# Optimization experiments

Measured on AMD Instinct MI355X. Metric: run time of the kernel, lower is better.

The kernel has to match this reference:

```python
import math
import jax, jax.numpy as jnp
import numpy as np

D_MODEL = 512
NHEAD = 8
D_HEAD = D_MODEL // NHEAD
TEMP = 0.8
B, LQ, LK = 16, 512, 1024
NEG = -1.0e9


def setup_inputs() -> dict:
    key = jax.random.key(0)
    ks = jax.random.split(key, 12)
    s = 1.0 / math.sqrt(D_MODEL)
    return {
        "Q_src": jax.random.normal(ks[0], (B, LQ, D_MODEL), jnp.float32),
        "KV_src": jax.random.normal(ks[1], (B, LK, D_MODEL), jnp.float32),
        "key_gate": jax.random.uniform(ks[2], (B, LK), jnp.float32, 1e-3, 1.0),
        "key_padding_mask": jax.random.randint(ks[3], (B, LK), 0, 2, jnp.int32),
        "Wq": jax.random.normal(ks[4], (D_MODEL, D_MODEL), jnp.float32) * s,
        "bq": jnp.zeros((D_MODEL,), jnp.float32),
        "Wk": jax.random.normal(ks[5], (D_MODEL, D_MODEL), jnp.float32) * s,
        "bk": jnp.zeros((D_MODEL,), jnp.float32),
        "Wv": jax.random.normal(ks[6], (D_MODEL, D_MODEL), jnp.float32) * s,
        "bv": jnp.zeros((D_MODEL,), jnp.float32),
        "Wo": jax.random.normal(ks[7], (D_MODEL, D_MODEL), jnp.float32) * s,
        "bo": jnp.zeros((D_MODEL,), jnp.float32),
    }


def reference(Q_src, KV_src, key_gate, key_padding_mask, Wq, bq, Wk, bk, Wv, bv, Wo, bo):
    b, lq, _ = Q_src.shape
    lk = KV_src.shape[1]
    # projections -> [B, H, L, Dh]
    q = (Q_src @ Wq + bq).reshape(b, lq, NHEAD, D_HEAD).transpose(0, 2, 1, 3)
    k = (KV_src @ Wk + bk).reshape(b, lk, NHEAD, D_HEAD).transpose(0, 2, 1, 3)
    v = (KV_src @ Wv + bv).reshape(b, lk, NHEAD, D_HEAD).transpose(0, 2, 1, 3)
    # scores with log-gate bias [B, H, Lq, Lk]
    logits = jnp.einsum("bhqd,bhkd->bhqk", q, k) / math.sqrt(D_HEAD)
    logits = logits + jnp.log(key_gate)[:, None, None, :]
    pad = (key_padding_mask == 0)[:, None, None, :]
    logits = jnp.where(pad, NEG, logits) / TEMP
    attn = jax.nn.softmax(logits, axis=-1)
    ctx = jnp.einsum("bhqk,bhkd->bhqd", attn, v)
    ctx = ctx.transpose(0, 2, 1, 3).reshape(b, lq, D_MODEL)
    return ctx @ Wo + bo
```

## Files before the change

kernel.cpp:

```cpp
#include <hip/hip_runtime.h>
#include <math.h>

typedef __bf16 bf16;
typedef __bf16 bf16x8 __attribute__((ext_vector_type(8)));
typedef __bf16 bf16x4 __attribute__((ext_vector_type(4)));
typedef __bf16 bf16x2 __attribute__((ext_vector_type(2)));
typedef float  f32x4  __attribute__((ext_vector_type(4)));
typedef unsigned int uint;

#define SCQ 0.15625f

#define VMC(n) asm volatile("s_waitcnt vmcnt(" #n ")" ::: "memory")
#define BARR do { __builtin_amdgcn_s_barrier(); __builtin_amdgcn_sched_barrier(0); } while (0)

__device__ __forceinline__ void gload16(const void* g, void* l) {
  __builtin_amdgcn_global_load_lds((const __attribute__((address_space(1))) void*)g,
                                   (__attribute__((address_space(3))) void*)l, 16, 0, 0);
}

__device__ __forceinline__ uint pk2(float a, float b) {
  bf16x2 t = {(bf16)a, (bf16)b};
  return __builtin_bit_cast(uint, t);
}

union V8 { bf16x8 v; bf16x4 h[2]; uint u[4]; };

__global__ void prep_k(const float* __restrict__ Wq, const float* __restrict__ Wk,
                       const float* __restrict__ Wv, const float* __restrict__ Wo,
                       bf16* __restrict__ Tq, bf16* __restrict__ Tkv, bf16* __restrict__ To,
                       const float* __restrict__ gate, const int* __restrict__ mask,
                       float* __restrict__ gfac) {
  const int bid = blockIdx.x, tid = threadIdx.x;
  if (bid < 256) {
    const int w = bid >> 6, t = bid & 63;
    const float* W = (w == 0) ? Wq : (w == 1) ? Wk : (w == 2) ? Wv : Wo;
    bf16* T = (w == 0) ? Tq : (w == 3) ? To : Tkv;
    const int ro = (w == 2) ? 512 : 0;
    const int k0 = (t >> 3) * 64, n0 = (t & 7) * 64;
    __shared__ bf16 tl[64][72];
#pragma unroll
    for (int i = 0; i < 16; i++) {
      int s = i * 256 + tid;
      int r = s >> 6, c = s & 63;
      tl[r][c] = (bf16)W[(size_t)(k0 + r) * 512 + n0 + c];
    }
    __syncthreads();
#pragma unroll
    for (int i = 0; i < 16; i++) {
      int s = i * 256 + tid;
      int r = s >> 6, c = s & 63;
      T[(size_t)(ro + n0 + r) * 512 + k0 + c] = tl[c][r];
    }
  } else {
    int i = (bid - 256) * 256 + tid;
    gfac[i] = mask[i] ? __expf(1.25f * __logf(gate[i])) : 0.0f;
  }
}

__global__ void conv_k(const float* __restrict__ s, bf16* __restrict__ d) {
  const size_t i = ((size_t)blockIdx.x * 256 + threadIdx.x) * 8;
  f32x4 a = *(const f32x4*)(s + i);
  f32x4 b = *(const f32x4*)(s + i + 4);
  bf16x8 o = {(bf16)a[0], (bf16)a[1], (bf16)a[2], (bf16)a[3],
              (bf16)b[0], (bf16)b[1], (bf16)b[2], (bf16)b[3]};
  *(bf16x8*)(d + i) = o;
}

__global__ __launch_bounds__(512, 2) void gemm_kv8(
    const bf16* __restrict__ A, const bf16* __restrict__ Bt,
    const float* __restrict__ kb, const float* __restrict__ vb,
    const float* __restrict__ gfac, bf16* __restrict__ K_out, bf16* __restrict__ V_out) {
  const int tid = threadIdx.x, w = tid >> 6, l = tid & 63;
  const int lg = l >> 4, lr = l & 15;
  const int bid = (int)(blockIdx.x & 7) * 32 + (int)(blockIdx.x >> 3);
  const int bm = (bid >> 2) * 256;
  const int bn = (bid & 3) * 256;
  const int wm = w >> 2, wn = w & 3;

  __shared__ __align__(16) bf16 AB[2][16384];

  const int lrow = l >> 2;
  const int cs = (l & 3) ^ ((l >> 3) & 3);

  f32x4 acc[8][4];
#pragma unroll
  for (int i = 0; i < 8; i++)
#pragma unroll
    for (int j = 0; j < 4; j++) acc[i][j] = (f32x4){0.f, 0.f, 0.f, 0.f};

  auto stA = [&](int p, int u, int kt) {
    const int rb = (w >> 2) * 128 + u * 64 + (w & 3) * 16;
    gload16(A + (size_t)(bm + rb + lrow) * 512 + kt * 32 + cs * 8, &AB[p][rb * 32]);
  };
  auto stB = [&](int p, int u, int kt) {
    const int rb = (w >> 1) * 64 + u * 32 + (w & 1) * 16;
    gload16(Bt + (size_t)(bn + rb + lrow) * 512 + kt * 32 + cs * 8, &AB[p][8192 + rb * 32]);
  };

  bf16x8 aA[4], bb0[2], bb1[2];
#define RDA(p, mh)                                                                   \
  _Pragma("unroll") for (int m2 = 0; m2 < 4; m2++) {                                 \
    const int row = wm * 128 + (mh) * 64 + m2 * 16 + lr;                             \
    aA[m2] = *(const bf16x8*)(&AB[p][row * 32 + ((lg ^ ((row >> 1) & 3)) * 8)]);     \
  }
#define RDB(p, nh, dst)                                                              \
  _Pragma("unroll") for (int n2 = 0; n2 < 2; n2++) {                                 \
    const int row = wn * 64 + (nh) * 32 + n2 * 16 + lr;                              \
    dst[n2] = *(const bf16x8*)(&AB[p][8192 + row * 32 + ((lg ^ ((row >> 1) & 3)) * 8)]); \
  }
#define MM(mh, nh, bbv)                                                              \
  __builtin_amdgcn_s_setprio(1);                                                     \
  _Pragma("unroll") for (int m2 = 0; m2 < 4; m2++)                                   \
  _Pragma("unroll") for (int n2 = 0; n2 < 2; n2++)                                   \
    acc[(mh) * 4 + m2][(nh) * 2 + n2] =                                              \
        __builtin_amdgcn_mfma_f32_16x16x32_bf16(aA[m2], bbv[n2],                     \
                                                acc[(mh) * 4 + m2][(nh) * 2 + n2], 0, 0, 0); \
  __builtin_amdgcn_s_setprio(0);

  stA(0, 0, 0); stB(0, 0, 0); stA(0, 1, 0); stB(0, 1, 0);
  stA(1, 0, 1); stB(1, 0, 1);
  VMC(4);
  BARR;

  for (int i = 0; i < 8; ++i) {
    const bool last = (i == 7);
    const int k1 = 2 * i + 1, k2 = 2 * i + 2, k3 = 2 * i + 3;
    stA(1, 1, k1); stB(1, 1, k1);
    RDA(0, 0); RDB(0, 0, bb0);
    MM(0, 0, bb0);
    VMC(4); BARR;
    RDB(0, 1, bb1);
    MM(0, 1, bb1);
    BARR;
    if (!last) stA(0, 0, k2);
    RDA(0, 1);
    MM(1, 0, bb0);
    BARR;
    if (!last) stB(0, 0, k2);
    MM(1, 1, bb1);
    if (last) { VMC(2); } else { VMC(4); }
    BARR;
    if (!last) { stA(0, 1, k2); stB(0, 1, k2); }
    RDA(1, 0); RDB(1, 0, bb0);
    MM(0, 0, bb0);
    if (last) { VMC(0); } else { VMC(4); }
    BARR;
    RDB(1, 1, bb1);
    MM(0, 1, bb1);
    BARR;
    if (!last) stA(1, 0, k3);
    RDA(1, 1);
    MM(1, 0, bb0);
    BARR;
    if (!last) stB(1, 0, k3);
    MM(1, 1, bb1);
    VMC(4); BARR;
  }
#undef RDA
#undef RDB
#undef MM

  if (bn < 512) {
#pragma unroll
    for (int mf = 0; mf < 8; mf++) {
#pragma unroll
      for (int nf = 0; nf < 4; nf++) {
        f32x4 c = acc[mf][nf];
        const int n = bn + wn * 64 + nf * 16 + lr;
        const int m0 = bm + wm * 128 + mf * 16 + lg * 4;
        const float bias = kb[n];
#pragma unroll
        for (int r = 0; r < 4; r++) K_out[(size_t)(m0 + r) * 512 + n] = (bf16)(c[r] + bias);
      }
    }
  } else {
#pragma unroll
    for (int mf = 0; mf < 8; mf++) {
#pragma unroll
      for (int nf = 0; nf < 4; nf++) {
        f32x4 c = acc[mf][nf];
        const int n = bn + wn * 64 + nf * 16 + lr;
        const int m0 = bm + wm * 128 + mf * 16 + lg * 4;
        const int nn = n - 512;
        const int hh = nn >> 6, dd = nn & 63;
        const int bb = m0 >> 10, key = m0 & 1023;
        const int u = key & 31;
        const int keyp = (key & ~31) + ((u & 15) >> 2) * 8 + ((u >> 4) & 1) * 4;
        const float bias = vb[nn];
        f32x4 g4 = *(const f32x4*)(gfac + m0);
        bf16x4 w4 = {(bf16)((c[0] + bias) * g4[0]), (bf16)((c[1] + bias) * g4[1]),
                     (bf16)((c[2] + bias) * g4[2]), (bf16)((c[3] + bias) * g4[3])};
        *(bf16x4*)(V_out + ((size_t)((bb * 8 + hh) * 64 + dd)) * 1024 + keyp) = w4;
      }
    }
  }
}

template <int BM, int OM, int NT, int CHUNK>
__global__ __launch_bounds__(256) void gemm_k(
    const bf16* __restrict__ A, const bf16* __restrict__ Bt,
    const float* __restrict__ b0, void* __restrict__ C0, float scale) {
  constexpr int MF = BM / 32;
  const int tid = threadIdx.x, w = tid >> 6, l = tid & 63;
  const int lg = l >> 4, lr = l & 15;
  const int bid = (int)(blockIdx.x & 7) * CHUNK + (int)(blockIdx.x >> 3);
  const int bm = (bid / NT) * BM;
  const int bn = (bid % NT) * 128;
  const int wr = (w >> 1) * (BM / 2), wc = (w & 1) * 64;
  __shared__ __align__(16) bf16 As[2][BM][64];
  __shared__ __align__(16) bf16 Bs[2][128][64];
  const int srow8 = l >> 3;
  const int c8 = (l & 7) ^ srow8;
  const int xorlr = (lr & 7);

  f32x4 acc[MF][4];
#pragma unroll
  for (int i = 0; i < MF; i++)
#pragma unroll
    for (int j = 0; j < 4; j++) acc[i][j] = (f32x4){0.f, 0.f, 0.f, 0.f};

  auto stage = [&](int buf, int k0) {
#pragma unroll
    for (int i = 0; i < MF; i++)
      gload16(A + (size_t)(bm + i * 32 + w * 8 + srow8) * 512 + k0 + c8 * 8,
              &As[buf][i * 32 + w * 8][0]);
#pragma unroll
    for (int i = 0; i < 4; i++)
      gload16(Bt + (size_t)(bn + i * 32 + w * 8 + srow8) * 512 + k0 + c8 * 8,
              &Bs[buf][i * 32 + w * 8][0]);
  };

  stage(0, 0);
  for (int t = 0; t < 8; ++t) {
    const int buf = t & 1;
    __syncthreads();
    if (t < 7) stage(buf ^ 1, (t + 1) * 64);
#pragma unroll
    for (int kk = 0; kk < 2; kk++) {
      bf16x8 af[MF], bfr[4];
#pragma unroll
      for (int mf = 0; mf < MF; mf++)
        af[mf] = *(const bf16x8*)(&As[buf][wr + mf * 16 + lr][((kk * 4 + lg) ^ xorlr) * 8]);
#pragma unroll
      for (int nf = 0; nf < 4; nf++)
        bfr[nf] = *(const bf16x8*)(&Bs[buf][wc + nf * 16 + lr][((kk * 4 + lg) ^ xorlr) * 8]);
#pragma unroll
      for (int mf = 0; mf < MF; mf++)
#pragma unroll
        for (int nf = 0; nf < 4; nf++)
          acc[mf][nf] = __builtin_amdgcn_mfma_f32_16x16x32_bf16(af[mf], bfr[nf], acc[mf][nf], 0, 0, 0);
    }
  }

#pragma unroll
  for (int mf = 0; mf < MF; mf++) {
#pragma unroll
    for (int nf = 0; nf < 4; nf++) {
      f32x4 c = acc[mf][nf];
      const int n = bn + wc + nf * 16 + lr;
      const int m0 = bm + wr + mf * 16 + lg * 4;
      const float bias = b0[n];
      if constexpr (OM == 0) {
        bf16* C = (bf16*)C0;
#pragma unroll
        for (int r = 0; r < 4; r++) C[(size_t)(m0 + r) * 512 + n] = (bf16)((c[r] + bias) * scale);
      } else {
        float* C = (float*)C0;
#pragma unroll
        for (int r = 0; r < 4; r++) C[(size_t)(m0 + r) * 512 + n] = c[r] + bias;
      }
    }
  }
}

__global__ __launch_bounds__(512) void attn_k(
    const bf16* __restrict__ Q, const bf16* __restrict__ Kb,
    const bf16* __restrict__ Vt, const float* __restrict__ gfac,
    bf16* __restrict__ ctx) {
  const int tid = threadIdx.x, w = tid >> 6, l = tid & 63;
  const int lg = l >> 4, lr = l & 15;
  const int bid = (int)(blockIdx.x & 7) * 32 + (int)(blockIdx.x >> 3);
  const int qb = bid & 1, h = (bid >> 1) & 7, b = bid >> 4;
  const int q0 = qb * 256;

  __shared__ __align__(16) bf16 Ks[2][64][64];
  __shared__ __align__(16) bf16 Vs[2][64][64];

  bf16x8 qf[2][2];
#pragma unroll
  for (int s = 0; s < 2; s++) {
    const bf16* qp = Q + (size_t)(b * 512 + q0 + w * 32 + s * 16 + lr) * 512 + h * 64;
    qf[s][0] = *(const bf16x8*)(qp + lg * 8);
    qf[s][1] = *(const bf16x8*)(qp + 32 + lg * 8);
  }

  f32x4 o[2][4];
#pragma unroll
  for (int s = 0; s < 2; s++)
#pragma unroll
    for (int i = 0; i < 4; i++) o[s][i] = (f32x4){0.f, 0.f, 0.f, 0.f};
  float m_r[2] = {-3.0e38f, -3.0e38f}, l_p[2] = {0.f, 0.f};
  const float* gfb = gfac + b * 1024;

  const int srow = w * 8 + (l >> 3);
  const int c8g = (l & 7) ^ ((l >> 3) & 7);
  const bf16* Kbase = Kb + ((size_t)b * 1024) * 512 + h * 64 + c8g * 8;
  const bf16* Vbase = Vt + (((size_t)(b * 8 + h)) * 64 + srow) * 1024 + c8g * 8;

  gload16(Kbase + (size_t)srow * 512, &Ks[0][w * 8][0]);
  gload16(Vbase, &Vs[0][w * 8][0]);

  for (int t = 0; t < 16; ++t) {
    const int buf = t & 1;
    __syncthreads();
    if (t < 15) {
      gload16(Kbase + (size_t)((t + 1) * 64 + srow) * 512, &Ks[buf ^ 1][w * 8][0]);
      gload16(Vbase + (t + 1) * 64, &Vs[buf ^ 1][w * 8][0]);
    }
    f32x4 gv[4];
#pragma unroll
    for (int f = 0; f < 4; f++) gv[f] = *(const f32x4*)(gfb + t * 64 + f * 16 + lg * 4);

    f32x4 s4[2][4];
    __builtin_amdgcn_s_setprio(1);
#pragma unroll
    for (int f = 0; f < 4; f++) {
      const int row = f * 16 + lr;
      const bf16x8 k0 = *(const bf16x8*)(&Ks[buf][row][(lg ^ (row & 7)) * 8]);
      const bf16x8 k1 = *(const bf16x8*)(&Ks[buf][row][((4 + lg) ^ (row & 7)) * 8]);
#pragma unroll
      for (int s = 0; s < 2; s++) {
        f32x4 z = (f32x4){0.f, 0.f, 0.f, 0.f};
        z = __builtin_amdgcn_mfma_f32_16x16x32_bf16(k0, qf[s][0], z, 0, 0, 0);
        s4[s][f] = __builtin_amdgcn_mfma_f32_16x16x32_bf16(k1, qf[s][1], z, 0, 0, 0);
      }
    }
    __builtin_amdgcn_s_setprio(0);

    V8 pb[2][2];
#pragma unroll
    for (int s = 0; s < 2; s++) {
      float mx = fmaxf(fmaxf(fmaxf(s4[s][0][0], s4[s][0][1]), fmaxf(s4[s][0][2], s4[s][0][3])),
                       fmaxf(fmaxf(s4[s][1][0], s4[s][1][1]), fmaxf(s4[s][1][2], s4[s][1][3])));
      mx = fmaxf(mx, fmaxf(fmaxf(fmaxf(s4[s][2][0], s4[s][2][1]), fmaxf(s4[s][2][2], s4[s][2][3])),
                           fmaxf(fmaxf(s4[s][3][0], s4[s][3][1]), fmaxf(s4[s][3][2], s4[s][3][3]))));
      mx = fmaxf(mx, __shfl_xor(mx, 16));
      mx = fmaxf(mx, __shfl_xor(mx, 32));
      if (!__all(mx <= m_r[s] + 8.f)) {
        const float mn = fmaxf(m_r[s], mx);
        const float al = __expf(m_r[s] - mn);
        m_r[s] = mn;
        l_p[s] *= al;
#pragma unroll
        for (int od = 0; od < 4; od++)
#pragma unroll
          for (int r = 0; r < 4; r++) o[s][od][r] *= al;
      }
      float p[4][4];
#pragma unroll
      for (int f = 0; f < 4; f++)
#pragma unroll
        for (int r = 0; r < 4; r++) p[f][r] = __expf(s4[s][f][r] - m_r[s]);
#pragma unroll
      for (int f = 0; f < 4; f++)
#pragma unroll
        for (int r = 0; r < 4; r++) l_p[s] = fmaf(p[f][r], gv[f][r], l_p[s]);
      pb[s][0].u[0] = pk2(p[0][0], p[0][1]); pb[s][0].u[1] = pk2(p[0][2], p[0][3]);
      pb[s][0].u[2] = pk2(p[1][0], p[1][1]); pb[s][0].u[3] = pk2(p[1][2], p[1][3]);
      pb[s][1].u[0] = pk2(p[2][0], p[2][1]); pb[s][1].u[1] = pk2(p[2][2], p[2][3]);
      pb[s][1].u[2] = pk2(p[3][0], p[3][1]); pb[s][1].u[3] = pk2(p[3][2], p[3][3]);
    }

    __builtin_amdgcn_s_setprio(1);
#pragma unroll
    for (int od = 0; od < 4; od++) {
      const int row = od * 16 + lr;
      const bf16x8 va0 = *(const bf16x8*)(&Vs[buf][row][(lg ^ (row & 7)) * 8]);
      const bf16x8 va1 = *(const bf16x8*)(&Vs[buf][row][((4 + lg) ^ (row & 7)) * 8]);
#pragma unroll
      for (int s = 0; s < 2; s++) {
        o[s][od] = __builtin_amdgcn_mfma_f32_16x16x32_bf16(va0, pb[s][0].v, o[s][od], 0, 0, 0);
        o[s][od] = __builtin_amdgcn_mfma_f32_16x16x32_bf16(va1, pb[s][1].v, o[s][od], 0, 0, 0);
      }
    }
    __builtin_amdgcn_s_setprio(0);
  }

#pragma unroll
  for (int s = 0; s < 2; s++) {
    float lp = l_p[s];
    lp += __shfl_xor(lp, 16);
    lp += __shfl_xor(lp, 32);
    const float inv = 1.0f / lp;
    bf16* cp = ctx + (size_t)(b * 512 + q0 + w * 32 + s * 16 + lr) * 512 + h * 64;
#pragma unroll
    for (int od = 0; od < 4; od++)
#pragma unroll
      for (int r = 0; r < 4; r++) cp[od * 16 + lg * 4 + r] = (bf16)(o[s][od][r] * inv);
  }
}

extern "C" void kernel_launch(void* const* d_in, const int* in_sizes, int n_in,
                              void* d_out, int out_size, void* d_ws, size_t ws_size,
                              hipStream_t stream) {
  (void)in_sizes; (void)n_in; (void)out_size; (void)ws_size;
  const float* Q_src = (const float*)d_in[0];
  const float* KV_src = (const float*)d_in[1];
  const float* gate = (const float*)d_in[2];
  const int* mask = (const int*)d_in[3];
  const float* Wq = (const float*)d_in[4];
  const float* bq = (const float*)d_in[5];
  const float* Wk = (const float*)d_in[6];
  const float* bk = (const float*)d_in[7];
  const float* Wv = (const float*)d_in[8];
  const float* bv = (const float*)d_in[9];
  const float* Wo = (const float*)d_in[10];
  const float* bo = (const float*)d_in[11];
  float* out = (float*)d_out;

  char* ws = (char*)d_ws;
  size_t off = 0;
  auto alloc = [&](size_t bytes) {
    char* p = ws + off;
    off += (bytes + 255) & ~(size_t)255;
    return p;
  };
  bf16* Wtq = (bf16*)alloc(512 * 512 * 2);
  bf16* Btkv = (bf16*)alloc(1024 * 512 * 2);
  bf16* Wto = (bf16*)alloc(512 * 512 * 2);
  float* gfac = (float*)alloc(16384 * 4);
  bf16* Qsb = (bf16*)alloc((size_t)8192 * 512 * 2);
  bf16* KVb = (bf16*)alloc((size_t)16384 * 512 * 2);
  bf16* Qb = (bf16*)alloc((size_t)8192 * 512 * 2);
  bf16* Kb = (bf16*)alloc((size_t)16384 * 512 * 2);
  bf16* Vt = (bf16*)alloc((size_t)16384 * 512 * 2);
  bf16* Cx = KVb;

  prep_k<<<320, 256, 0, stream>>>(Wq, Wk, Wv, Wo, Wtq, Btkv, Wto, gate, mask, gfac);
  conv_k<<<2048, 256, 0, stream>>>(Q_src, Qsb);
  conv_k<<<4096, 256, 0, stream>>>(KV_src, KVb);
  gemm_kv8<<<256, 512, 0, stream>>>(KVb, Btkv, bk, bv, gfac, Kb, Vt);
  gemm_k<64, 0, 4, 64><<<512, 256, 0, stream>>>(Qsb, Wtq, bq, Qb, SCQ);
  attn_k<<<256, 512, 0, stream>>>(Qb, Kb, Vt, gfac, Cx);
  gemm_k<64, 2, 4, 64><<<512, 256, 0, stream>>>(Cx, Wto, bo, out, 1.0f);
}
```

Baseline: 98.05 us.

## Fuse conversion kernels into prep, triple-buffer GEMM and attention, use exp2 softmax

```diff
diff --git a/kernel.cpp b/kernel.cpp
--- a/kernel.cpp
+++ b/kernel.cpp
@@ -8,10 +8,16 @@
 typedef float  f32x4  __attribute__((ext_vector_type(4)));
 typedef unsigned int uint;
 
-#define SCQ 0.15625f
+#define SCQ2 0.22542110f
 
 #define VMC(n) asm volatile("s_waitcnt vmcnt(" #n ")" ::: "memory")
 #define BARR do { __builtin_amdgcn_s_barrier(); __builtin_amdgcn_sched_barrier(0); } while (0)
+
+#if __has_builtin(__builtin_amdgcn_exp2f)
+#define EXP2F __builtin_amdgcn_exp2f
+#else
+#define EXP2F exp2f
+#endif
 
 __device__ __forceinline__ void gload16(const void* g, void* l) {
   __builtin_amdgcn_global_load_lds((const __attribute__((address_space(1))) void*)g,
@@ -29,7 +35,9 @@
                        const float* __restrict__ Wv, const float* __restrict__ Wo,
                        bf16* __restrict__ Tq, bf16* __restrict__ Tkv, bf16* __restrict__ To,
                        const float* __restrict__ gate, const int* __restrict__ mask,
-                       float* __restrict__ gfac) {
+                       float* __restrict__ gfac,
+                       const float* __restrict__ Qs, const float* __restrict__ KVs,
+                       bf16* __restrict__ Qsb, bf16* __restrict__ KVb) {
   const int bid = blockIdx.x, tid = threadIdx.x;
   if (bid < 256) {
     const int w = bid >> 6, t = bid & 63;
@@ -51,19 +59,21 @@
       int r = s >> 6, c = s & 63;
       T[(size_t)(ro + n0 + r) * 512 + k0 + c] = tl[c][r];
     }
-  } else {
+  } else if (bid < 320) {
     int i = (bid - 256) * 256 + tid;
     gfac[i] = mask[i] ? __expf(1.25f * __logf(gate[i])) : 0.0f;
-  }
-}
-
-__global__ void conv_k(const float* __restrict__ s, bf16* __restrict__ d) {
-  const size_t i = ((size_t)blockIdx.x * 256 + threadIdx.x) * 8;
-  f32x4 a = *(const f32x4*)(s + i);
-  f32x4 b = *(const f32x4*)(s + i + 4);
-  bf16x8 o = {(bf16)a[0], (bf16)a[1], (bf16)a[2], (bf16)a[3],
-              (bf16)b[0], (bf16)b[1], (bf16)b[2], (bf16)b[3]};
-  *(bf16x8*)(d + i) = o;
+  } else {
+    const float* s;
+    bf16* d;
+    size_t i;
+    if (bid < 2368) { s = Qs; d = Qsb; i = ((size_t)(bid - 320) * 256 + tid) * 8; }
+    else            { s = KVs; d = KVb; i = ((size_t)(bid - 2368) * 256 + tid) * 8; }
+    f32x4 a = *(const f32x4*)(s + i);
+    f32x4 b = *(const f32x4*)(s + i + 4);
+    bf16x8 o = {(bf16)a[0], (bf16)a[1], (bf16)a[2], (bf16)a[3],
+                (bf16)b[0], (bf16)b[1], (bf16)b[2], (bf16)b[3]};
+    *(bf16x8*)(d + i) = o;
+  }
 }
 
 __global__ __launch_bounds__(512, 2) void gemm_kv8(
@@ -196,64 +206,64 @@
   }
 }
 
-template <int BM, int OM, int NT, int CHUNK>
-__global__ __launch_bounds__(256) void gemm_k(
+template <int OM, int NT, int CHUNK>
+__global__ __launch_bounds__(256, 2) void gemm_k(
     const bf16* __restrict__ A, const bf16* __restrict__ Bt,
     const float* __restrict__ b0, void* __restrict__ C0, float scale) {
-  constexpr int MF = BM / 32;
   const int tid = threadIdx.x, w = tid >> 6, l = tid & 63;
   const int lg = l >> 4, lr = l & 15;
   const int bid = (int)(blockIdx.x & 7) * CHUNK + (int)(blockIdx.x >> 3);
-  const int bm = (bid / NT) * BM;
+  const int bm = (bid / NT) * 64;
   const int bn = (bid % NT) * 128;
-  const int wr = (w >> 1) * (BM / 2), wc = (w & 1) * 64;
-  __shared__ __align__(16) bf16 As[2][BM][64];
-  __shared__ __align__(16) bf16 Bs[2][128][64];
-  const int srow8 = l >> 3;
-  const int c8 = (l & 7) ^ srow8;
-  const int xorlr = (lr & 7);
-
-  f32x4 acc[MF][4];
-#pragma unroll
-  for (int i = 0; i < MF; i++)
+  const int wr = (w >> 1) * 32, wc = (w & 1) * 64;
+  __shared__ __align__(16) bf16 As[3][64][32];
+  __shared__ __align__(16) bf16 Bs[3][128][32];
+  const int r16 = l >> 2;
+  const int cs = (l & 3) ^ ((l >> 3) & 3);
+
+  f32x4 acc[2][4];
+#pragma unroll
+  for (int i = 0; i < 2; i++)
 #pragma unroll
     for (int j = 0; j < 4; j++) acc[i][j] = (f32x4){0.f, 0.f, 0.f, 0.f};
 
-  auto stage = [&](int buf, int k0) {
-#pragma unroll
-    for (int i = 0; i < MF; i++)
-      gload16(A + (size_t)(bm + i * 32 + w * 8 + srow8) * 512 + k0 + c8 * 8,
-              &As[buf][i * 32 + w * 8][0]);
-#pragma unroll
-    for (int i = 0; i < 4; i++)
-      gload16(Bt + (size_t)(bn + i * 32 + w * 8 + srow8) * 512 + k0 + c8 * 8,
-              &Bs[buf][i * 32 + w * 8][0]);
+  auto stage = [&](int buf, int kt) {
+    gload16(A + (size_t)(bm + w * 16 + r16) * 512 + kt * 32 + cs * 8, &As[buf][w * 16][0]);
+#pragma unroll
+    for (int j = 0; j < 2; j++)
+      gload16(Bt + (size_t)(bn + w * 32 + j * 16 + r16) * 512 + kt * 32 + cs * 8,
+              &Bs[buf][w * 32 + j * 16][0]);
   };
 
   stage(0, 0);
-  for (int t = 0; t < 8; ++t) {
-    const int buf = t & 1;
-    __syncthreads();
-    if (t < 7) stage(buf ^ 1, (t + 1) * 64);
-#pragma unroll
-    for (int kk = 0; kk < 2; kk++) {
-      bf16x8 af[MF], bfr[4];
-#pragma unroll
-      for (int mf = 0; mf < MF; mf++)
-        af[mf] = *(const bf16x8*)(&As[buf][wr + mf * 16 + lr][((kk * 4 + lg) ^ xorlr) * 8]);
+  stage(1, 1);
+  for (int t = 0; t < 16; ++t) {
+    const int buf = t % 3;
+    if (t == 15) { VMC(0); } else { VMC(3); }
+    BARR;
+    if (t < 14) stage((t + 2) % 3, t + 2);
+    bf16x8 af[2], bfr[4];
+#pragma unroll
+    for (int mf = 0; mf < 2; mf++) {
+      const int row = wr + mf * 16 + lr;
+      af[mf] = *(const bf16x8*)(&As[buf][row][(lg ^ ((row >> 1) & 3)) * 8]);
+    }
+#pragma unroll
+    for (int nf = 0; nf < 4; nf++) {
+      const int row = wc + nf * 16 + lr;
+      bfr[nf] = *(const bf16x8*)(&Bs[buf][row][(lg ^ ((row >> 1) & 3)) * 8]);
+    }
+    __builtin_amdgcn_s_setprio(1);
+#pragma unroll
+    for (int mf = 0; mf < 2; mf++)
 #pragma unroll
       for (int nf = 0; nf < 4; nf++)
-        bfr[nf] = *(const bf16x8*)(&Bs[buf][wc + nf * 16 + lr][((kk * 4 + lg) ^ xorlr) * 8]);
-#pragma unroll
-      for (int mf = 0; mf < MF; mf++)
-#pragma unroll
-        for (int nf = 0; nf < 4; nf++)
-          acc[mf][nf] = __builtin_amdgcn_mfma_f32_16x16x32_bf16(af[mf], bfr[nf], acc[mf][nf], 0, 0, 0);
-    }
-  }
-
-#pragma unroll
-  for (int mf = 0; mf < MF; mf++) {
+        acc[mf][nf] = __builtin_amdgcn_mfma_f32_16x16x32_bf16(af[mf], bfr[nf], acc[mf][nf], 0, 0, 0);
+    __builtin_amdgcn_s_setprio(0);
+  }
+
+#pragma unroll
+  for (int mf = 0; mf < 2; mf++) {
 #pragma unroll
     for (int nf = 0; nf < 4; nf++) {
       f32x4 c = acc[mf][nf];
@@ -273,18 +283,19 @@
   }
 }
 
-__global__ __launch_bounds__(512) void attn_k(
+__global__ __launch_bounds__(256, 2) void attn_k(
     const bf16* __restrict__ Q, const bf16* __restrict__ Kb,
     const bf16* __restrict__ Vt, const float* __restrict__ gfac,
     bf16* __restrict__ ctx) {
   const int tid = threadIdx.x, w = tid >> 6, l = tid & 63;
   const int lg = l >> 4, lr = l & 15;
-  const int bid = (int)(blockIdx.x & 7) * 32 + (int)(blockIdx.x >> 3);
-  const int qb = bid & 1, h = (bid >> 1) & 7, b = bid >> 4;
-  const int q0 = qb * 256;
-
-  __shared__ __align__(16) bf16 Ks[2][64][64];
-  __shared__ __align__(16) bf16 Vs[2][64][64];
+  const int bid = (int)(blockIdx.x & 7) * 64 + (int)(blockIdx.x >> 3);
+  const int qb = bid & 3, h = (bid >> 2) & 7, b = bid >> 5;
+  const int q0 = qb * 128;
+
+  __shared__ __align__(16) bf16 Ks[3][64][64];
+  __shared__ __align__(16) bf16 Vs[3][64][64];
+  __shared__ __align__(16) float gfs[1024];
 
   bf16x8 qf[2][2];
 #pragma unroll
@@ -299,27 +310,35 @@
   for (int s = 0; s < 2; s++)
 #pragma unroll
     for (int i = 0; i < 4; i++) o[s][i] = (f32x4){0.f, 0.f, 0.f, 0.f};
-  float m_r[2] = {-3.0e38f, -3.0e38f}, l_p[2] = {0.f, 0.f};
-  const float* gfb = gfac + b * 1024;
-
-  const int srow = w * 8 + (l >> 3);
+  float m_r[2] = {-3.0e38f, -3.0e38f};
+  f32x4 lacc[2] = {(f32x4){0.f, 0.f, 0.f, 0.f}, (f32x4){0.f, 0.f, 0.f, 0.f}};
+
+  const int r8 = l >> 3;
   const int c8g = (l & 7) ^ ((l >> 3) & 7);
   const bf16* Kbase = Kb + ((size_t)b * 1024) * 512 + h * 64 + c8g * 8;
-  const bf16* Vbase = Vt + (((size_t)(b * 8 + h)) * 64 + srow) * 1024 + c8g * 8;
-
-  gload16(Kbase + (size_t)srow * 512, &Ks[0][w * 8][0]);
-  gload16(Vbase, &Vs[0][w * 8][0]);
+  const bf16* Vbase = Vt + ((size_t)(b * 8 + h) * 64) * 1024 + c8g * 8;
+
+  auto stage = [&](int buf, int t) {
+    const int kv0 = t * 64;
+    gload16(Kbase + (size_t)(kv0 + w * 16 + r8) * 512, &Ks[buf][w * 16][0]);
+    gload16(Kbase + (size_t)(kv0 + w * 16 + 8 + r8) * 512, &Ks[buf][w * 16 + 8][0]);
+    gload16(Vbase + (size_t)(w * 16 + r8) * 1024 + kv0, &Vs[buf][w * 16][0]);
+    gload16(Vbase + (size_t)(w * 16 + 8 + r8) * 1024 + kv0, &Vs[buf][w * 16 + 8][0]);
+  };
+
+  gload16(gfac + b * 1024 + w * 256 + l * 4, &gfs[w * 256]);
+  stage(0, 0);
+  stage(1, 1);
 
   for (int t = 0; t < 16; ++t) {
-    const int buf = t & 1;
-    __syncthreads();
-    if (t < 15) {
-      gload16(Kbase + (size_t)((t + 1) * 64 + srow) * 512, &Ks[buf ^ 1][w * 8][0]);
-      gload16(Vbase + (t + 1) * 64, &Vs[buf ^ 1][w * 8][0]);
-    }
-    f32x4 gv[4];
-#pragma unroll
-    for (int f = 0; f < 4; f++) gv[f] = *(const f32x4*)(gfb + t * 64 + f * 16 + lg * 4);
+    const int buf = t % 3;
+    if (t == 15) { VMC(0); } else { VMC(4); }
+    BARR;
+    if (t < 14) stage((t + 2) % 3, t + 2);
+
+    f32x4 gvv[4];
+#pragma unroll
+    for (int f = 0; f < 4; f++) gvv[f] = *(const f32x4*)(&gfs[t * 64 + f * 16 + lg * 4]);
 
     f32x4 s4[2][4];
     __builtin_amdgcn_s_setprio(1);
@@ -340,17 +359,17 @@
     V8 pb[2][2];
 #pragma unroll
     for (int s = 0; s < 2; s++) {
-      float mx = fmaxf(fmaxf(fmaxf(s4[s][0][0], s4[s][0][1]), fmaxf(s4[s][0][2], s4[s][0][3])),
-                       fmaxf(fmaxf(s4[s][1][0], s4[s][1][1]), fmaxf(s4[s][1][2], s4[s][1][3])));
-      mx = fmaxf(mx, fmaxf(fmaxf(fmaxf(s4[s][2][0], s4[s][2][1]), fmaxf(s4[s][2][2], s4[s][2][3])),
-                           fmaxf(fmaxf(s4[s][3][0], s4[s][3][1]), fmaxf(s4[s][3][2], s4[s][3][3]))));
+      f32x4 m01 = __builtin_elementwise_max(s4[s][0], s4[s][1]);
+      f32x4 m23 = __builtin_elementwise_max(s4[s][2], s4[s][3]);
+      f32x4 m4 = __builtin_elementwise_max(m01, m23);
+      float mx = fmaxf(fmaxf(m4[0], m4[1]), fmaxf(m4[2], m4[3]));
       mx = fmaxf(mx, __shfl_xor(mx, 16));
       mx = fmaxf(mx, __shfl_xor(mx, 32));
-      if (!__all(mx <= m_r[s] + 8.f)) {
+      if (!__all(mx <= m_r[s] + 11.5f)) {
         const float mn = fmaxf(m_r[s], mx);
-        const float al = __expf(m_r[s] - mn);
+        const float al = EXP2F(m_r[s] - mn);
         m_r[s] = mn;
-        l_p[s] *= al;
+        lacc[s] *= al;
 #pragma unroll
         for (int od = 0; od < 4; od++)
 #pragma unroll
@@ -360,11 +379,11 @@
 #pragma unroll
       for (int f = 0; f < 4; f++)
 #pragma unroll
-        for (int r = 0; r < 4; r++) p[f][r] = __expf(s4[s][f][r] - m_r[s]);
+        for (int r = 0; r < 4; r++) p[f][r] = EXP2F(s4[s][f][r] - m_r[s]);
 #pragma unroll
       for (int f = 0; f < 4; f++)
 #pragma unroll
-        for (int r = 0; r < 4; r++) l_p[s] = fmaf(p[f][r], gv[f][r], l_p[s]);
+        for (int r = 0; r < 4; r++) lacc[s][r] = fmaf(p[f][r], gvv[f][r], lacc[s][r]);
       pb[s][0].u[0] = pk2(p[0][0], p[0][1]); pb[s][0].u[1] = pk2(p[0][2], p[0][3]);
       pb[s][0].u[2] = pk2(p[1][0], p[1][1]); pb[s][0].u[3] = pk2(p[1][2], p[1][3]);
       pb[s][1].u[0] = pk2(p[2][0], p[2][1]); pb[s][1].u[1] = pk2(p[2][2], p[2][3]);
@@ -388,7 +407,7 @@
 
 #pragma unroll
   for (int s = 0; s < 2; s++) {
-    float lp = l_p[s];
+    float lp = (lacc[s][0] + lacc[s][1]) + (lacc[s][2] + lacc[s][3]);
     lp += __shfl_xor(lp, 16);
     lp += __shfl_xor(lp, 32);
     const float inv = 1.0f / lp;
@@ -436,11 +455,10 @@
   bf16* Vt = (bf16*)alloc((size_t)16384 * 512 * 2);
   bf16* Cx = KVb;
 
-  prep_k<<<320, 256, 0, stream>>>(Wq, Wk, Wv, Wo, Wtq, Btkv, Wto, gate, mask, gfac);
-  conv_k<<<2048, 256, 0, stream>>>(Q_src, Qsb);
-  conv_k<<<4096, 256, 0, stream>>>(KV_src, KVb);
+  prep_k<<<6464, 256, 0, stream>>>(Wq, Wk, Wv, Wo, Wtq, Btkv, Wto, gate, mask, gfac,
+                                   Q_src, KV_src, Qsb, KVb);
   gemm_kv8<<<256, 512, 0, stream>>>(KVb, Btkv, bk, bv, gfac, Kb, Vt);
-  gemm_k<64, 0, 4, 64><<<512, 256, 0, stream>>>(Qsb, Wtq, bq, Qb, SCQ);
-  attn_k<<<256, 512, 0, stream>>>(Qb, Kb, Vt, gfac, Cx);
-  gemm_k<64, 2, 4, 64><<<512, 256, 0, stream>>>(Cx, Wto, bo, out, 1.0f);
-}
+  gemm_k<0, 4, 64><<<512, 256, 0, stream>>>(Qsb, Wtq, bq, Qb, SCQ2);
+  attn_k<<<512, 256, 0, stream>>>(Qb, Kb, Vt, gfac, Cx);
+  gemm_k<2, 4, 64><<<512, 256, 0, stream>>>(Cx, Wto, bo, out, 1.0f);
+}
```

After: 90.26 us. 1.09x faster.
